# Performance work log

Hardware: AMD Instinct MI355X
Metric: run time of the kernel (lower is better)

Reference implementation:

```python
import math
import jax, jax.numpy as jnp
import numpy as np

N, C, H = 64, 512, 512
SHIFT = 2  # frozen stand-in for random.randint(-3, 3) at module init


def setup_inputs() -> dict:
    key = jax.random.key(0)
    k1, k2, k3 = jax.random.split(key, 3)
    x = jax.random.normal(k1, (N, C, H), dtype=jnp.float32)
    bound = math.sqrt(3.0 / C)
    p1_w = jax.random.uniform(k2, (C, 1), dtype=jnp.float32, minval=-bound, maxval=bound)
    p7_w = 0.02 * jax.random.truncated_normal(k3, -2.0, 2.0, (1, C, H), dtype=jnp.float32)
    return {"x": x, "p1_w": p1_w, "p7_w": p7_w}


def reference(x, p1_w, p7_w):
    n, c, h = x.shape
    inv_sc = 1.0 / math.sqrt(c)
    inv_sh = 1.0 / math.sqrt(h)
    # t1: einsum('abc,bd->adc') with d=1, flattened to (n,h)
    t1 = jnp.einsum('nch,c->nh', x, p1_w[:, 0])
    t2 = jnp.roll(x, SHIFT, axis=1)
    t3 = t1[:, None, :] + t2                     # (n,c,h)
    t4 = x * t3
    t5 = jax.nn.relu(x)
    t7 = p7_w * t5                               # (n,c,h)
    # t8 = softmax(t5^T @ x / sqrt(c))           (n,h,h)
    t8 = jax.nn.softmax(jnp.einsum('nch,ncg->nhg', t5, x) * inv_sc, axis=-1)
    # t9 = t5 @ t4^T / sqrt(h)                   (n,c,c)
    t9 = jnp.einsum('nch,ndh->ncd', t5, t4) * inv_sh
    # t10 = softmax(t7 @ t3^T / sqrt(h))         (n,c,c); (c//g,g) view is cosmetic
    t10 = jax.nn.softmax(jnp.einsum('nch,ndh->ncd', t7, t3) * inv_sh, axis=-1)
    t11 = jnp.minimum(t4, x)
    # t12 = t9^T @ t7 / sqrt(c)                  (n,c,h)
    t12 = jnp.einsum('ndi,ndh->nih', t9, t7) * inv_sc
    # t13 = t11^T @ t2 / sqrt(c)                 (n,h,h)
    t13 = jnp.einsum('nch,ncg->nhg', t11, t2) * inv_sc
    # t14 = softmax(t9^T @ t10^T / sqrt(c))      (n,c,c)
    t14 = jax.nn.softmax(jnp.einsum('nki,njk->nij', t9, t10) * inv_sc, axis=-1)
    # t15 = softmax(t13 @ t8 / sqrt(h))          (n,h,h)
    t15 = jax.nn.softmax(jnp.einsum('nij,njk->nik', t13, t8) * inv_sh, axis=-1)
    # t16 = t12^T @ t14^T / sqrt(c)              (n,h,c)
    t16 = jnp.einsum('nkh,njk->nhj', t12, t14) * inv_sc
    # t17 = t16^T @ t15 / sqrt(h)                (n,c,h)
    t17 = jnp.einsum('nkc,nkj->ncj', t16, t15) * inv_sh
    return t17
```

## Files before the change

kernel.cpp:

```cpp
#include <hip/hip_runtime.h>
#include <math.h>

namespace {

constexpr int kC = 512;
constexpr int kH = 512;
constexpr int kN = 64;
constexpr int kMat = kC * kH;
constexpr float kInvS = 0.04419417382415922f;

enum { SRC_RAW = 0, SRC_X, SRC_T2, SRC_T3, SRC_T4, SRC_T5, SRC_T7, SRC_T11 };

using bf16x8 = __attribute__((ext_vector_type(8))) __bf16;
using f32x4  = __attribute__((ext_vector_type(4))) float;

__device__ __forceinline__ float4 ld4(const float* p) {
  return *reinterpret_cast<const float4*>(p);
}

template <int SRC>
__device__ __forceinline__ float4 elem4(const float* __restrict__ raw,
                                        const float* __restrict__ x,
                                        const float* __restrict__ t1,
                                        const float* __restrict__ p7,
                                        int n, int r, int s) {
  const int nb = n * kMat;
  if constexpr (SRC == SRC_RAW) {
    return ld4(raw + nb + r * kH + s);
  } else if constexpr (SRC == SRC_X) {
    return ld4(x + nb + r * kH + s);
  } else if constexpr (SRC == SRC_T5) {
    float4 v = ld4(x + nb + r * kH + s);
    return make_float4(fmaxf(v.x, 0.f), fmaxf(v.y, 0.f),
                       fmaxf(v.z, 0.f), fmaxf(v.w, 0.f));
  } else if constexpr (SRC == SRC_T7) {
    float4 v = ld4(x + nb + r * kH + s);
    float4 p = ld4(p7 + r * kH + s);
    return make_float4(p.x * fmaxf(v.x, 0.f), p.y * fmaxf(v.y, 0.f),
                       p.z * fmaxf(v.z, 0.f), p.w * fmaxf(v.w, 0.f));
  } else {
    const int rr = (r + kC - 2) & (kC - 1);
    float4 xr = ld4(x + nb + rr * kH + s);
    if constexpr (SRC == SRC_T2) return xr;
    float4 tv = ld4(t1 + n * kH + s);
    float4 t3 = make_float4(tv.x + xr.x, tv.y + xr.y, tv.z + xr.z, tv.w + xr.w);
    if constexpr (SRC == SRC_T3) return t3;
    float4 xv = ld4(x + nb + r * kH + s);
    float4 t4 = make_float4(xv.x * t3.x, xv.y * t3.y, xv.z * t3.z, xv.w * t3.w);
    if constexpr (SRC == SRC_T4) return t4;
    return make_float4(fminf(t4.x, xv.x), fminf(t4.y, xv.y),
                       fminf(t4.z, xv.z), fminf(t4.w, xv.w));
  }
}

__device__ __forceinline__ unsigned cvtpk(float lo, float hi) {
  unsigned r;
  asm("v_cvt_pk_bf16_f32 %0, %1, %2" : "=v"(r) : "v"(lo), "v"(hi));
  return r;
}

__device__ __forceinline__ void split2(float a, float b, unsigned& q0,
                                       unsigned& q1, unsigned& q2) {
  q0 = cvtpk(a, b);
  float a0 = __builtin_bit_cast(float, q0 << 16);
  float b0 = __builtin_bit_cast(float, q0 & 0xFFFF0000u);
  float ra = a - a0, rb = b - b0;
  q1 = cvtpk(ra, rb);
  float a1 = __builtin_bit_cast(float, q1 << 16);
  float b1 = __builtin_bit_cast(float, q1 & 0xFFFF0000u);
  q2 = cvtpk(ra - a1, rb - b1);
}

constexpr int kRowS = 40;
constexpr int kPlane = 128 * kRowS;
constexpr int kMatS = 3 * kPlane;

__device__ __forceinline__ void store3(unsigned short* dst, int off,
                                       unsigned p0a, unsigned p0b,
                                       unsigned p1a, unsigned p1b,
                                       unsigned p2a, unsigned p2b) {
  *reinterpret_cast<uint2*>(dst + off)              = make_uint2(p0a, p0b);
  *reinterpret_cast<uint2*>(dst + kPlane + off)     = make_uint2(p1a, p1b);
  *reinterpret_cast<uint2*>(dst + 2 * kPlane + off) = make_uint2(p2a, p2b);
}

template <int SRC, bool TRANS>
__device__ __forceinline__ void stage_tile(unsigned short* dst,
                                           const float* __restrict__ raw,
                                           const float* __restrict__ x,
                                           const float* __restrict__ t1,
                                           const float* __restrict__ p7,
                                           int n, int r0, int k0, int tid) {
  if constexpr (!TRANS) {
#pragma unroll
    for (int i = 0; i < 4; ++i) {
      int e = tid + i * 256;
      int row = e >> 3;
      int k4 = (e & 7) << 2;
      float4 v = elem4<SRC>(raw, x, t1, p7, n, r0 + row, k0 + k4);
      unsigned p0a, p1a, p2a, p0b, p1b, p2b;
      split2(v.x, v.y, p0a, p1a, p2a);
      split2(v.z, v.w, p0b, p1b, p2b);
      store3(dst, row * kRowS + k4, p0a, p0b, p1a, p1b, p2a, p2b);
    }
  } else {
    int kb = tid >> 5;
    int mb = tid & 31;
    float4 v[4];
#pragma unroll
    for (int j = 0; j < 4; ++j)
      v[j] = elem4<SRC>(raw, x, t1, p7, n, k0 + kb * 4 + j, r0 + mb * 4);
    const float* vf = reinterpret_cast<const float*>(v);
#pragma unroll
    for (int i = 0; i < 4; ++i) {
      unsigned p0a, p1a, p2a, p0b, p1b, p2b;
      split2(vf[0 * 4 + i], vf[1 * 4 + i], p0a, p1a, p2a);
      split2(vf[2 * 4 + i], vf[3 * 4 + i], p0b, p1b, p2b);
      store3(dst, (mb * 4 + i) * kRowS + kb * 4, p0a, p0b, p1a, p1b, p2a, p2b);
    }
  }
}

template <int ASRC, int AT, int BSRC, int BT>
__global__ __launch_bounds__(256, 2) void gemm_kernel(
    const float* __restrict__ Araw, const float* __restrict__ Braw,
    const float* __restrict__ x, const float* __restrict__ t1,
    const float* __restrict__ p7, float* __restrict__ C, float alpha) {
  __shared__ unsigned short smem[2 * kMatS];
  const int n = blockIdx.z;
  const int i0 = blockIdx.y * 128;
  const int j0 = blockIdx.x * 128;
  const int tid = threadIdx.x;
  const int lane = tid & 63;
  const int wid = tid >> 6;
  const int wr = wid >> 1, wc = wid & 1;

  f32x4 acc[4][4];
#pragma unroll
  for (int a = 0; a < 4; ++a)
#pragma unroll
    for (int b = 0; b < 4; ++b) acc[a][b] = (f32x4)0.f;

  const int frow = lane & 15;
  const int kq = (lane >> 4) * 8;

  for (int k0 = 0; k0 < kC; k0 += 32) {
    __syncthreads();
    stage_tile<ASRC, AT == 1>(smem, Araw, x, t1, p7, n, i0, k0, tid);
    stage_tile<BSRC, BT == 0>(smem + kMatS, Braw, x, t1, p7, n, j0, k0, tid);
    __syncthreads();

    bf16x8 B0[4], B1[4], B2[4];
#pragma unroll
    for (int nj = 0; nj < 4; ++nj) {
      int off = kMatS + (wc * 64 + nj * 16 + frow) * kRowS + kq;
      B0[nj] = *reinterpret_cast<const bf16x8*>(smem + off);
      B1[nj] = *reinterpret_cast<const bf16x8*>(smem + kPlane + off);
      B2[nj] = *reinterpret_cast<const bf16x8*>(smem + 2 * kPlane + off);
    }
#pragma unroll
    for (int mi = 0; mi < 4; ++mi) {
      int off = (wr * 64 + mi * 16 + frow) * kRowS + kq;
      bf16x8 A0 = *reinterpret_cast<const bf16x8*>(smem + off);
      bf16x8 A1 = *reinterpret_cast<const bf16x8*>(smem + kPlane + off);
      bf16x8 A2 = *reinterpret_cast<const bf16x8*>(smem + 2 * kPlane + off);
#pragma unroll
      for (int nj = 0; nj < 4; ++nj) {
        f32x4 c = acc[mi][nj];
        c = __builtin_amdgcn_mfma_f32_16x16x32_bf16(A1, B1[nj], c, 0, 0, 0);
        c = __builtin_amdgcn_mfma_f32_16x16x32_bf16(A0, B2[nj], c, 0, 0, 0);
        c = __builtin_amdgcn_mfma_f32_16x16x32_bf16(A2, B0[nj], c, 0, 0, 0);
        c = __builtin_amdgcn_mfma_f32_16x16x32_bf16(A0, B1[nj], c, 0, 0, 0);
        c = __builtin_amdgcn_mfma_f32_16x16x32_bf16(A1, B0[nj], c, 0, 0, 0);
        c = __builtin_amdgcn_mfma_f32_16x16x32_bf16(A0, B0[nj], c, 0, 0, 0);
        acc[mi][nj] = c;
      }
    }
  }

  const int nb = n * kMat;
  const int rbase = (lane >> 4) * 4;
#pragma unroll
  for (int mi = 0; mi < 4; ++mi) {
#pragma unroll
    for (int nj = 0; nj < 4; ++nj) {
      int row0 = i0 + wr * 64 + mi * 16 + rbase;
      int col = j0 + wc * 64 + nj * 16 + frow;
      float* cp = C + nb + row0 * kH + col;
#pragma unroll
      for (int r = 0; r < 4; ++r) cp[r * kH] = acc[mi][nj][r] * alpha;
    }
  }
}

__global__ __launch_bounds__(256) void t1_kernel(const float* __restrict__ x,
                                                 const float* __restrict__ w,
                                                 float* __restrict__ t1) {
  int idx = blockIdx.x * 256 + threadIdx.x;
  int n = idx >> 9;
  const float* xp = x + n * kMat + (idx & (kH - 1));
  float s = 0.f;
#pragma unroll 8
  for (int c = 0; c < kC; ++c) s = fmaf(xp[c * kH], w[c], s);
  t1[idx] = s;
}

__global__ __launch_bounds__(256) void softmax_kernel(float* __restrict__ buf) {
  __shared__ float red[8];
  float* p = buf + (size_t)blockIdx.x * kH;
  int t = threadIdx.x;
  float2 v = reinterpret_cast<float2*>(p)[t];
  float m = fmaxf(v.x, v.y);
#pragma unroll
  for (int o = 32; o; o >>= 1) m = fmaxf(m, __shfl_xor(m, o));
  if ((t & 63) == 0) red[t >> 6] = m;
  __syncthreads();
  m = fmaxf(fmaxf(red[0], red[1]), fmaxf(red[2], red[3]));
  float e0 = expf(v.x - m), e1 = expf(v.y - m);
  float s = e0 + e1;
#pragma unroll
  for (int o = 32; o; o >>= 1) s += __shfl_xor(s, o);
  __syncthreads();
  if ((t & 63) == 0) red[4 + (t >> 6)] = s;
  __syncthreads();
  s = red[4] + red[5] + red[6] + red[7];
  float inv = 1.f / s;
  reinterpret_cast<float2*>(p)[t] = make_float2(e0 * inv, e1 * inv);
}

}

extern "C" void kernel_launch(void* const* d_in, const int* in_sizes, int n_in,
                              void* d_out, int out_size, void* d_ws,
                              size_t ws_size, hipStream_t stream) {
  (void)in_sizes; (void)n_in; (void)out_size;
  const float* x  = (const float*)d_in[0];
  const float* w  = (const float*)d_in[1];
  const float* p7 = (const float*)d_in[2];
  float* out = (float*)d_out;

  const size_t BUF = (size_t)kN * kMat;
  const size_t need = (4 * BUF + (size_t)kN * kH) * sizeof(float);
  float* ws = (float*)d_ws;
  if (ws_size < need) {
    static float* g_extra = nullptr;
    if (!g_extra) (void)hipMalloc((void**)&g_extra, need);
    ws = g_extra;
  }
  float* b0 = ws;
  float* b1 = b0 + BUF;
  float* b2 = b1 + BUF;
  float* b3 = b2 + BUF;
  float* t1 = b3 + BUF;

  dim3 gg(4, 4, kN);
  dim3 bb(256);
  const int rows = kN * kH;

  t1_kernel<<<rows / 256, bb, 0, stream>>>(x, w, t1);

  gemm_kernel<SRC_T5, 0, SRC_T4, 1><<<gg, bb, 0, stream>>>(nullptr, nullptr, x, t1, p7, b0, kInvS);
  gemm_kernel<SRC_T7, 0, SRC_T3, 1><<<gg, bb, 0, stream>>>(nullptr, nullptr, x, t1, p7, b1, kInvS);
  softmax_kernel<<<rows, bb, 0, stream>>>(b1);
  gemm_kernel<SRC_RAW, 1, SRC_RAW, 1><<<gg, bb, 0, stream>>>(b0, b1, x, t1, p7, b2, kInvS);
  softmax_kernel<<<rows, bb, 0, stream>>>(b2);
  gemm_kernel<SRC_RAW, 1, SRC_T7, 0><<<gg, bb, 0, stream>>>(b0, nullptr, x, t1, p7, b1, kInvS);
  gemm_kernel<SRC_RAW, 1, SRC_RAW, 1><<<gg, bb, 0, stream>>>(b1, b2, x, t1, p7, b0, kInvS);
  gemm_kernel<SRC_T11, 1, SRC_T2, 0><<<gg, bb, 0, stream>>>(nullptr, nullptr, x, t1, p7, b1, kInvS);
  gemm_kernel<SRC_T5, 1, SRC_X, 0><<<gg, bb, 0, stream>>>(nullptr, nullptr, x, t1, p7, b2, kInvS);
  softmax_kernel<<<rows, bb, 0, stream>>>(b2);
  gemm_kernel<SRC_RAW, 0, SRC_RAW, 0><<<gg, bb, 0, stream>>>(b1, b2, x, t1, p7, b3, kInvS);
  softmax_kernel<<<rows, bb, 0, stream>>>(b3);
  gemm_kernel<SRC_RAW, 1, SRC_RAW, 0><<<gg, bb, 0, stream>>>(b0, b3, x, t1, p7, out, kInvS);
}
```

Measured before the change: 1.348 ms.

## Swizzle LDS tile layout, use scalar coalesced transposed staging, raise occupancy

Replaces the padded 40-element LDS row stride with a dense 32-element layout that uses an XOR swizzle, so the bf16x8 fragment reads avoid bank conflicts without padding. This shrinks shared memory per block, and launch bounds are raised from 2 to 3 blocks per CU. The transposed staging path now loads scalar elements, strided by 32 columns per thread, so neighbouring threads read neighbouring addresses, and the LDS writes use the same swizzle. The costs are more scalar global loads in place of float4 loads, possible register pressure at the higher occupancy target, and swizzled stores that may still conflict.

After: 1.355 ms. No clear change (+0.5%).

```diff
diff --git a/kernel.cpp b/kernel.cpp
--- a/kernel.cpp
+++ b/kernel.cpp
@@ -53,6 +53,34 @@
   }
 }
 
+template <int SRC>
+__device__ __forceinline__ float elem1(const float* __restrict__ raw,
+                                       const float* __restrict__ x,
+                                       const float* __restrict__ t1,
+                                       const float* __restrict__ p7,
+                                       int n, int r, int s) {
+  const int nb = n * kMat;
+  if constexpr (SRC == SRC_RAW) {
+    return raw[nb + r * kH + s];
+  } else if constexpr (SRC == SRC_X) {
+    return x[nb + r * kH + s];
+  } else if constexpr (SRC == SRC_T5) {
+    return fmaxf(x[nb + r * kH + s], 0.f);
+  } else if constexpr (SRC == SRC_T7) {
+    return p7[r * kH + s] * fmaxf(x[nb + r * kH + s], 0.f);
+  } else {
+    const int rr = (r + kC - 2) & (kC - 1);
+    float xr = x[nb + rr * kH + s];
+    if constexpr (SRC == SRC_T2) return xr;
+    float t3 = t1[n * kH + s] + xr;
+    if constexpr (SRC == SRC_T3) return t3;
+    float xv = x[nb + r * kH + s];
+    float t4 = xv * t3;
+    if constexpr (SRC == SRC_T4) return t4;
+    return fminf(t4, xv);
+  }
+}
+
 __device__ __forceinline__ unsigned cvtpk(float lo, float hi) {
   unsigned r;
   asm("v_cvt_pk_bf16_f32 %0, %1, %2" : "=v"(r) : "v"(lo), "v"(hi));
@@ -71,14 +99,20 @@
   q2 = cvtpk(ra - a1, rb - b1);
 }
 
-constexpr int kRowS = 40;
-constexpr int kPlane = 128 * kRowS;
+constexpr int kPlane = 128 * 32;
 constexpr int kMatS = 3 * kPlane;
 
-__device__ __forceinline__ void store3(unsigned short* dst, int off,
+__device__ __forceinline__ int lds_addr(int r, int ku) {
+  int line = r >> 1;
+  int slot = ((r & 1) << 2) | (ku >> 3);
+  return (line << 6) + ((slot ^ (line & 7)) << 3) + (ku & 7);
+}
+
+__device__ __forceinline__ void store3(unsigned short* dst, int r, int ku,
                                        unsigned p0a, unsigned p0b,
                                        unsigned p1a, unsigned p1b,
                                        unsigned p2a, unsigned p2b) {
+  int off = lds_addr(r, ku);
   *reinterpret_cast<uint2*>(dst + off)              = make_uint2(p0a, p0b);
   *reinterpret_cast<uint2*>(dst + kPlane + off)     = make_uint2(p1a, p1b);
   *reinterpret_cast<uint2*>(dst + 2 * kPlane + off) = make_uint2(p2a, p2b);
@@ -101,28 +135,30 @@
       unsigned p0a, p1a, p2a, p0b, p1b, p2b;
       split2(v.x, v.y, p0a, p1a, p2a);
       split2(v.z, v.w, p0b, p1b, p2b);
-      store3(dst, row * kRowS + k4, p0a, p0b, p1a, p1b, p2a, p2b);
+      store3(dst, row, k4, p0a, p0b, p1a, p1b, p2a, p2b);
     }
   } else {
-    int kb = tid >> 5;
-    int mb = tid & 31;
-    float4 v[4];
+    const int kb = tid >> 5;
+    const int mb = tid & 31;
+    float v[4][4];
 #pragma unroll
     for (int j = 0; j < 4; ++j)
-      v[j] = elem4<SRC>(raw, x, t1, p7, n, k0 + kb * 4 + j, r0 + mb * 4);
-    const float* vf = reinterpret_cast<const float*>(v);
+#pragma unroll
+      for (int i = 0; i < 4; ++i)
+        v[j][i] = elem1<SRC>(raw, x, t1, p7, n, k0 + kb * 4 + j,
+                             r0 + mb + 32 * i);
 #pragma unroll
     for (int i = 0; i < 4; ++i) {
-      unsigned p0a, p1a, p2a, p0b, p1b, p2b;
-      split2(vf[0 * 4 + i], vf[1 * 4 + i], p0a, p1a, p2a);
-      split2(vf[2 * 4 + i], vf[3 * 4 + i], p0b, p1b, p2b);
-      store3(dst, (mb * 4 + i) * kRowS + kb * 4, p0a, p0b, p1a, p1b, p2a, p2b);
+      unsigned q0a, q1a, q2a, q0b, q1b, q2b;
+      split2(v[0][i], v[1][i], q0a, q1a, q2a);
+      split2(v[2][i], v[3][i], q0b, q1b, q2b);
+      store3(dst, mb + 32 * i, kb * 4, q0a, q0b, q1a, q1b, q2a, q2b);
     }
   }
 }
 
 template <int ASRC, int AT, int BSRC, int BT>
-__global__ __launch_bounds__(256, 2) void gemm_kernel(
+__global__ __launch_bounds__(256, 3) void gemm_kernel(
     const float* __restrict__ Araw, const float* __restrict__ Braw,
     const float* __restrict__ x, const float* __restrict__ t1,
     const float* __restrict__ p7, float* __restrict__ C, float alpha) {
@@ -153,14 +189,14 @@
     bf16x8 B0[4], B1[4], B2[4];
 #pragma unroll
     for (int nj = 0; nj < 4; ++nj) {
-      int off = kMatS + (wc * 64 + nj * 16 + frow) * kRowS + kq;
+      int off = kMatS + lds_addr(wc * 64 + nj * 16 + frow, kq);
       B0[nj] = *reinterpret_cast<const bf16x8*>(smem + off);
       B1[nj] = *reinterpret_cast<const bf16x8*>(smem + kPlane + off);
       B2[nj] = *reinterpret_cast<const bf16x8*>(smem + 2 * kPlane + off);
     }
 #pragma unroll
     for (int mi = 0; mi < 4; ++mi) {
-      int off = (wr * 64 + mi * 16 + frow) * kRowS + kq;
+      int off = lds_addr(wr * 64 + mi * 16 + frow, kq);
       bf16x8 A0 = *reinterpret_cast<const bf16x8*>(smem + off);
       bf16x8 A1 = *reinterpret_cast<const bf16x8*>(smem + kPlane + off);
       bf16x8 A2 = *reinterpret_cast<const bf16x8*>(smem + 2 * kPlane + off);
```
